# Optimization experiments

Hardware: AMD Instinct MI355X
Metric: run time of the kernel (lower is better)

Reference implementation:

```python
import jax, jax.numpy as jnp
import numpy as np


def phi(x):
    # ELU + 1 feature map (Katharopoulos et al. 2020)
    return jax.nn.elu(x) + 1.0


def setup_inputs() -> dict:
    key = jax.random.key(0)
    k1, k2, k3 = jax.random.split(key, 3)
    B, T, D = 2, 2048, 512
    x = jax.random.normal(k1, (B, T, D), dtype=jnp.float32)
    # torch nn.Linear stores weight as (out_features, in_features)
    w_qkv = jax.random.normal(k2, (3 * D, D), dtype=jnp.float32) * 0.02
    w_out = jax.random.normal(k3, (D, D), dtype=jnp.float32) * 0.02
    return {"x": x, "w_qkv": w_qkv, "w_out": w_out, "n_heads": 16}


def reference(x, w_qkv, w_out, n_heads):
    B, T, D = x.shape
    H = n_heads
    Dh = D // H
    qkv = x @ w_qkv.T                                   # (B,T,3D)
    qkv = qkv.reshape(B, T, 3, H, Dh).transpose(2, 0, 3, 1, 4)  # (3,B,H,T,Dh)
    q, k, v = phi(qkv[0]), phi(qkv[1]), qkv[2]
    # kv outer product: (B,H,T,Dh_k,Dh_v), causal cumsum over time
    kv = k[..., :, None] * v[..., None, :]
    kv_cumsum = jnp.cumsum(kv, axis=2)
    num = jnp.einsum('bhtd,bhtde->bhte', q, kv_cumsum)  # (B,H,T,Dh)
    k_cumsum = jnp.cumsum(k, axis=2)
    denom = jnp.einsum('bhtd,bhtd->bht', q, k_cumsum)[..., None]
    denom = jnp.maximum(denom, 1e-6)
    out = num / denom                                   # (B,H,T,Dh)
    out = out.transpose(0, 2, 1, 3).reshape(B, T, D)
    return out @ w_out.T
```

## Files before the change

### kernel.cpp

```cpp
#include <hip/hip_runtime.h>
#include <math.h>

#define B_ 2
#define T_ 2048
#define D_ 512
#define H_ 16
#define DH 32
#define L_ 64
#define C_ 32
#define BH 32
#define NC 1024
#define VTP 72

typedef __attribute__((ext_vector_type(8))) short bf16x8;
typedef __attribute__((ext_vector_type(4))) float f32x4;
typedef __attribute__((ext_vector_type(4))) unsigned short u16x4;

#define AS1 __attribute__((address_space(1)))
#define AS3 __attribute__((address_space(3)))

__device__ __forceinline__ float bf2f(unsigned short u) {
    union { float f; unsigned int i; } v; v.i = ((unsigned int)u) << 16; return v.f;
}
__device__ __forceinline__ unsigned short f2bf(float f) {
    union { float f; unsigned int u; } v; v.f = f;
    unsigned int u = v.u;
    unsigned int r = u + 0x7FFFu + ((u >> 16) & 1u);
    return (unsigned short)(r >> 16);
}
__device__ __forceinline__ bf16x8 phi_frag(bf16x8 in) {
    bf16x8 r;
    #pragma unroll
    for (int i = 0; i < 8; ++i) {
        float f = bf2f((unsigned short)in[i]);
        f = f > 0.f ? f + 1.f : __expf(f);
        r[i] = (short)f2bf(f);
    }
    return r;
}
__device__ __forceinline__ void gload_lds16(const unsigned short* g, unsigned short* l) {
    __builtin_amdgcn_global_load_lds((const AS1 unsigned int*)g, (AS3 unsigned int*)l, 16, 0, 0);
}

__global__ __launch_bounds__(256) void convert_all(const float* __restrict__ x,
                                                   const float* __restrict__ wq,
                                                   const float* __restrict__ wo,
                                                   unsigned short* __restrict__ xb,
                                                   unsigned short* __restrict__ wqb,
                                                   unsigned short* __restrict__ wob)
{
    int i = blockIdx.x * 256 + threadIdx.x;
    const float* src; unsigned short* dst; int off;
    if (i < 524288)      { src = x;  dst = xb;  off = i; }
    else if (i < 720896) { src = wq; dst = wqb; off = i - 524288; }
    else                 { src = wo; dst = wob; off = i - 720896; }
    float4 v = ((const float4*)src)[off];
    u16x4 o;
    o.x = f2bf(v.x); o.y = f2bf(v.y); o.z = f2bf(v.z); o.w = f2bf(v.w);
    ((u16x4*)dst)[off] = o;
}

template<bool OUT_BF16>
__global__ __launch_bounds__(256) void gemm_bf16_nt(const unsigned short* __restrict__ A,
                                                    const unsigned short* __restrict__ W,
                                                    void* __restrict__ Cout,
                                                    int M, int N, int K)
{
    __shared__ unsigned short As[128][32];
    __shared__ unsigned short Bs[128][32];
    const int tid = threadIdx.x;
    const int lane = tid & 63;
    const int wave = tid >> 6;
    const int wr = wave >> 1;
    const int wc = wave & 1;
    const size_t bm = (size_t)blockIdx.x * 128;
    const size_t bn = (size_t)blockIdx.y * 128;

    const int srow = wave * 32 + (lane >> 2);
    const int scol = (lane & 3) * 8;
    const unsigned short* ag0 = A + (bm + srow) * (size_t)K + scol;
    const unsigned short* ag1 = ag0 + (size_t)16 * K;
    const unsigned short* bg0 = W + (bn + srow) * (size_t)K + scol;
    const unsigned short* bg1 = bg0 + (size_t)16 * K;
    unsigned short* al0 = &As[wave * 32][0];
    unsigned short* al1 = &As[wave * 32 + 16][0];
    unsigned short* bl0 = &Bs[wave * 32][0];
    unsigned short* bl1 = &Bs[wave * 32 + 16][0];

    f32x4 acc[4][4];
    #pragma unroll
    for (int m = 0; m < 4; ++m)
        #pragma unroll
        for (int n = 0; n < 4; ++n)
            acc[m][n] = (f32x4){0.f, 0.f, 0.f, 0.f};

    const int rr = lane & 15;
    const int kb = (lane >> 4) * 8;

    for (int k0 = 0; k0 < K; k0 += 32) {
        gload_lds16(ag0 + k0, al0);
        gload_lds16(ag1 + k0, al1);
        gload_lds16(bg0 + k0, bl0);
        gload_lds16(bg1 + k0, bl1);
        __syncthreads();
        bf16x8 af[4], bfr[4];
        #pragma unroll
        for (int m = 0; m < 4; ++m) af[m] = *(const bf16x8*)&As[wr * 64 + m * 16 + rr][kb];
        #pragma unroll
        for (int n = 0; n < 4; ++n) bfr[n] = *(const bf16x8*)&Bs[wc * 64 + n * 16 + rr][kb];
        #pragma unroll
        for (int m = 0; m < 4; ++m)
            #pragma unroll
            for (int n = 0; n < 4; ++n)
                acc[m][n] = __builtin_amdgcn_mfma_f32_16x16x32_bf16(af[m], bfr[n], acc[m][n], 0, 0, 0);
        __syncthreads();
    }

    const int cr = (lane >> 4) * 4;
    const int cc = lane & 15;
    #pragma unroll
    for (int m = 0; m < 4; ++m)
        #pragma unroll
        for (int n = 0; n < 4; ++n)
            #pragma unroll
            for (int j = 0; j < 4; ++j) {
                size_t row = bm + wr * 64 + m * 16 + cr + j;
                size_t col = bn + wc * 64 + n * 16 + cc;
                float v = acc[m][n][j];
                if (OUT_BF16) ((unsigned short*)Cout)[row * N + col] = f2bf(v);
                else          ((float*)Cout)[row * N + col] = v;
            }
}

__global__ __launch_bounds__(256) void chunk_sum(const unsigned short* __restrict__ qkv,
                                                 float* __restrict__ cSf)
{
    __shared__ unsigned short Kt[4][DH][VTP];
    __shared__ unsigned short Vt[4][48][VTP];
    const int tid = threadIdx.x;
    const int lane = tid & 63;
    const int wave = tid >> 6;
    const int chunk = blockIdx.x * 4 + wave;
    const int c = chunk & 31;
    const int h = (chunk >> 5) & 15;
    const int b = chunk >> 9;
    const size_t rowbase = ((size_t)(b * T_ + c * L_)) * (3 * D_) + h * DH;
    const int half = lane & 1;

    #pragma unroll
    for (int it = 0; it < 2; ++it) {
        int t = (lane >> 1) + it * 32;
        const unsigned short* kp = qkv + rowbase + (size_t)t * (3 * D_) + D_ + half * 16;
        const unsigned short* vp = qkv + rowbase + (size_t)t * (3 * D_) + 2 * D_ + half * 16;
        bf16x8 k0 = phi_frag(*(const bf16x8*)kp);
        bf16x8 k1 = phi_frag(*(const bf16x8*)(kp + 8));
        bf16x8 v0 = *(const bf16x8*)vp;
        bf16x8 v1 = *(const bf16x8*)(vp + 8);
        #pragma unroll
        for (int i = 0; i < 8; ++i) {
            Kt[wave][half * 16 + i][t]     = (unsigned short)k0[i];
            Kt[wave][half * 16 + 8 + i][t] = (unsigned short)k1[i];
            Vt[wave][half * 16 + i][t]     = (unsigned short)v0[i];
            Vt[wave][half * 16 + 8 + i][t] = (unsigned short)v1[i];
        }
    }
    Vt[wave][32][lane] = 0x3F80;

    const int fr = lane & 15;
    const int fg = lane >> 4;
    f32x4 acc[3][2];
    #pragma unroll
    for (int m = 0; m < 3; ++m)
        #pragma unroll
        for (int n = 0; n < 2; ++n)
            acc[m][n] = (f32x4){0.f, 0.f, 0.f, 0.f};

    #pragma unroll
    for (int ks = 0; ks < 2; ++ks) {
        int toff = fg * 8 + ks * 32;
        bf16x8 av[3], bk[2];
        #pragma unroll
        for (int m = 0; m < 3; ++m) av[m] = *(const bf16x8*)&Vt[wave][m * 16 + fr][toff];
        #pragma unroll
        for (int n = 0; n < 2; ++n) bk[n] = *(const bf16x8*)&Kt[wave][n * 16 + fr][toff];
        #pragma unroll
        for (int m = 0; m < 3; ++m)
            #pragma unroll
            for (int n = 0; n < 2; ++n)
                acc[m][n] = __builtin_amdgcn_mfma_f32_16x16x32_bf16(av[m], bk[n], acc[m][n], 0, 0, 0);
    }

    float* outp = cSf + (size_t)chunk * (48 * 32);
    #pragma unroll
    for (int m = 0; m < 2; ++m)
        #pragma unroll
        for (int n = 0; n < 2; ++n)
            #pragma unroll
            for (int r = 0; r < 4; ++r)
                outp[(m * 16 + fg * 4 + r) * 32 + n * 16 + fr] = acc[m][n][r];
    if (fg == 0) {
        #pragma unroll
        for (int n = 0; n < 2; ++n)
            outp[32 * 32 + n * 16 + fr] = acc[2][n][0];
    }
}

__global__ __launch_bounds__(256) void chunk_scan(const float* __restrict__ cSf,
                                                  unsigned short* __restrict__ cSt)
{
    int idx = blockIdx.x * 256 + threadIdx.x;
    int bh = idx / (33 * 32);
    int r  = idx % (33 * 32);
    float acc = 0.f;
    const float* src = cSf + (size_t)bh * C_ * (48 * 32) + r;
    unsigned short* dst = cSt + (size_t)bh * C_ * (48 * 32) + r;
    #pragma unroll 8
    for (int c = 0; c < C_; ++c) {
        dst[(size_t)c * (48 * 32)] = f2bf(acc);
        acc += src[(size_t)c * (48 * 32)];
    }
}

__global__ __launch_bounds__(256) void chunk_out(const unsigned short* __restrict__ qkv,
                                                 const unsigned short* __restrict__ cSt,
                                                 unsigned short* __restrict__ attn)
{
    __shared__ unsigned short Vt[2][48][VTP];
    __shared__ unsigned short Am[4][32][VTP];
    const int tid = threadIdx.x;
    const int lane = tid & 63;
    const int wave = tid >> 6;
    const int ci = wave >> 1;
    const int wh = wave & 1;
    const int chunk = blockIdx.x * 2 + ci;
    const int c = chunk & 31;
    const int h = (chunk >> 5) & 15;
    const int b = chunk >> 9;
    const size_t rowbase = ((size_t)(b * T_ + c * L_)) * (3 * D_) + h * DH;
    const int fr = lane & 15;
    const int fg = lane >> 4;

    {
        int t = wh * 32 + (lane >> 1);
        int half = lane & 1;
        const unsigned short* vp = qkv + rowbase + (size_t)t * (3 * D_) + 2 * D_ + half * 16;
        bf16x8 v0 = *(const bf16x8*)vp;
        bf16x8 v1 = *(const bf16x8*)(vp + 8);
        #pragma unroll
        for (int i = 0; i < 8; ++i) {
            Vt[ci][half * 16 + i][t]     = (unsigned short)v0[i];
            Vt[ci][half * 16 + 8 + i][t] = (unsigned short)v1[i];
        }
        if (half == 0) Vt[ci][32][t] = 0x3F80;
    }

    bf16x8 aq[2];
    #pragma unroll
    for (int mm = 0; mm < 2; ++mm) {
        int m = wh * 2 + mm;
        const unsigned short* qp = qkv + rowbase + (size_t)(m * 16 + fr) * (3 * D_) + fg * 8;
        aq[mm] = phi_frag(*(const bf16x8*)qp);
    }
    bf16x8 bk[4];
    const int nmax = wh * 2 + 1;
    #pragma unroll
    for (int n = 0; n < 4; ++n) {
        if (n <= nmax) {
            const unsigned short* kp = qkv + rowbase + (size_t)(n * 16 + fr) * (3 * D_) + D_ + fg * 8;
            bk[n] = phi_frag(*(const bf16x8*)kp);
        }
    }
    bf16x8 bkv[3];
    #pragma unroll
    for (int n = 0; n < 3; ++n)
        bkv[n] = *(const bf16x8*)&cSt[(size_t)chunk * 1536 + (size_t)(n * 16 + fr) * 32 + fg * 8];

    f32x4 zero = (f32x4){0.f, 0.f, 0.f, 0.f};
    f32x4 acc[2][3];
    #pragma unroll
    for (int mm = 0; mm < 2; ++mm)
        #pragma unroll
        for (int n = 0; n < 3; ++n)
            acc[mm][n] = __builtin_amdgcn_mfma_f32_16x16x32_bf16(aq[mm], bkv[n], zero, 0, 0, 0);

    #pragma unroll
    for (int mm = 0; mm < 2; ++mm) {
        int m = wh * 2 + mm;
        #pragma unroll
        for (int n = 0; n < 4; ++n) {
            if (n <= m) {
                f32x4 s = __builtin_amdgcn_mfma_f32_16x16x32_bf16(aq[mm], bk[n], zero, 0, 0, 0);
                #pragma unroll
                for (int r = 0; r < 4; ++r) {
                    unsigned short v = f2bf(s[r]);
                    if (n == m && fr > fg * 4 + r) v = 0;
                    Am[wave][mm * 16 + fg * 4 + r][n * 16 + fr] = v;
                }
            }
        }
    }
    {
        int zc = wh ? 48 : 16;
        *(uint2*)&Am[wave][fr][zc + fg * 4] = (uint2){0u, 0u};
    }
    __syncthreads();

    #pragma unroll
    for (int ks = 0; ks < 2; ++ks) {
        if (ks <= wh) {
            bf16x8 bv[3];
            #pragma unroll
            for (int n = 0; n < 3; ++n)
                bv[n] = *(const bf16x8*)&Vt[ci][n * 16 + fr][fg * 8 + ks * 32];
            #pragma unroll
            for (int mm = 0; mm < 2; ++mm) {
                bf16x8 aa = *(const bf16x8*)&Am[wave][mm * 16 + fr][fg * 8 + ks * 32];
                #pragma unroll
                for (int n = 0; n < 3; ++n)
                    acc[mm][n] = __builtin_amdgcn_mfma_f32_16x16x32_bf16(aa, bv[n], acc[mm][n], 0, 0, 0);
            }
        }
    }

    #pragma unroll
    for (int mm = 0; mm < 2; ++mm) {
        float dn[4];
        #pragma unroll
        for (int r = 0; r < 4; ++r)
            dn[r] = __shfl(acc[mm][2][r], lane & 48);
        #pragma unroll
        for (int r = 0; r < 4; ++r) {
            float inv = 1.0f / fmaxf(dn[r], 1e-6f);
            #pragma unroll
            for (int n = 0; n < 2; ++n)
                Am[wave][mm * 16 + fg * 4 + r][n * 16 + fr] = f2bf(acc[mm][n][r] * inv);
        }
    }
    {
        int lrow = lane >> 1;
        int half = lane & 1;
        uint4 q0 = *(const uint4*)&Am[wave][lrow][half * 16];
        uint4 q1 = *(const uint4*)&Am[wave][lrow][half * 16 + 8];
        size_t grow = (size_t)(b * T_ + c * L_ + wh * 32 + lrow);
        unsigned short* dst = attn + grow * D_ + h * DH + half * 16;
        *(uint4*)dst = q0;
        *(uint4*)(dst + 8) = q1;
    }
}

extern "C" void kernel_launch(void* const* d_in, const int* in_sizes, int n_in,
                              void* d_out, int out_size, void* d_ws, size_t ws_size,
                              hipStream_t stream) {
    const float* x     = (const float*)d_in[0];
    const float* w_qkv = (const float*)d_in[1];
    const float* w_out = (const float*)d_in[2];
    float* out = (float*)d_out;

    char* ws = (char*)d_ws;
    unsigned short* qkvb  = (unsigned short*)ws;
    unsigned short* attnb = (unsigned short*)(ws + 12582912);
    unsigned short* xb    = (unsigned short*)(ws + 16777216);
    unsigned short* wqb   = (unsigned short*)(ws + 20971520);
    unsigned short* wob   = (unsigned short*)(ws + 22544384);
    float* cSf            = (float*)(ws + 23068672);
    unsigned short* cSt   = (unsigned short*)(ws + 29360128);

    convert_all<<<3072, 256, 0, stream>>>(x, w_qkv, w_out, xb, wqb, wob);

    dim3 g1(4096 / 128, 1536 / 128);
    gemm_bf16_nt<true><<<g1, 256, 0, stream>>>(xb, wqb, qkvb, 4096, 1536, 512);

    chunk_sum<<<NC / 4, 256, 0, stream>>>(qkvb, cSf);
    chunk_scan<<<132, 256, 0, stream>>>(cSf, cSt);
    chunk_out<<<NC / 2, 256, 0, stream>>>(qkvb, cSt, attnb);

    dim3 g2(4096 / 128, 512 / 128);
    gemm_bf16_nt<false><<<g2, 256, 0, stream>>>(attnb, wob, out, 4096, 512, 512);
}
```

Baseline: 55.50 us.

## Fuse chunk prefix scan into chunk_out and use 64-row tiles for output GEMM

Removes the separate chunk_scan kernel: each chunk_out wave now sums the preceding chunks' fp32 state directly from cSf before converting to bf16, trading one launch and a bf16 staging buffer for redundant O(c) reads per chunk. The GEMM is templated on the M tile size, and the output projection uses BM=64, which doubles its block count (256 instead of 128) to fill more CUs. The redundant prefix reads grow with chunk index, so late chunks do up to 31 extra state loads.

```diff
diff --git a/kernel.cpp b/kernel.cpp
--- a/kernel.cpp
+++ b/kernel.cpp
@@ -60,36 +60,35 @@
     ((u16x4*)dst)[off] = o;
 }
 
-template<bool OUT_BF16>
+template<int BM, bool OUT_BF16>
 __global__ __launch_bounds__(256) void gemm_bf16_nt(const unsigned short* __restrict__ A,
                                                     const unsigned short* __restrict__ W,
                                                     void* __restrict__ Cout,
                                                     int M, int N, int K)
 {
-    __shared__ unsigned short As[128][32];
+    constexpr int MF = BM / 32;
+    __shared__ unsigned short As[BM][32];
     __shared__ unsigned short Bs[128][32];
     const int tid = threadIdx.x;
     const int lane = tid & 63;
     const int wave = tid >> 6;
     const int wr = wave >> 1;
     const int wc = wave & 1;
-    const size_t bm = (size_t)blockIdx.x * 128;
+    const size_t bm = (size_t)blockIdx.x * BM;
     const size_t bn = (size_t)blockIdx.y * 128;
 
-    const int srow = wave * 32 + (lane >> 2);
-    const int scol = (lane & 3) * 8;
-    const unsigned short* ag0 = A + (bm + srow) * (size_t)K + scol;
-    const unsigned short* ag1 = ag0 + (size_t)16 * K;
-    const unsigned short* bg0 = W + (bn + srow) * (size_t)K + scol;
+    const int lrow = lane >> 2;
+    const int lcol = (lane & 3) * 8;
+    const unsigned short* ag0 = A + (bm + wave * (BM / 4) + lrow) * (size_t)K + lcol;
+    unsigned short* al0 = &As[wave * (BM / 4)][0];
+    const unsigned short* bg0 = W + (bn + wave * 32 + lrow) * (size_t)K + lcol;
     const unsigned short* bg1 = bg0 + (size_t)16 * K;
-    unsigned short* al0 = &As[wave * 32][0];
-    unsigned short* al1 = &As[wave * 32 + 16][0];
     unsigned short* bl0 = &Bs[wave * 32][0];
     unsigned short* bl1 = &Bs[wave * 32 + 16][0];
 
-    f32x4 acc[4][4];
-    #pragma unroll
-    for (int m = 0; m < 4; ++m)
+    f32x4 acc[MF][4];
+    #pragma unroll
+    for (int m = 0; m < MF; ++m)
         #pragma unroll
         for (int n = 0; n < 4; ++n)
             acc[m][n] = (f32x4){0.f, 0.f, 0.f, 0.f};
@@ -99,17 +98,17 @@
 
     for (int k0 = 0; k0 < K; k0 += 32) {
         gload_lds16(ag0 + k0, al0);
-        gload_lds16(ag1 + k0, al1);
+        if constexpr (BM == 128) gload_lds16(ag0 + (size_t)16 * K + k0, al0 + 16 * 32);
         gload_lds16(bg0 + k0, bl0);
         gload_lds16(bg1 + k0, bl1);
         __syncthreads();
-        bf16x8 af[4], bfr[4];
-        #pragma unroll
-        for (int m = 0; m < 4; ++m) af[m] = *(const bf16x8*)&As[wr * 64 + m * 16 + rr][kb];
+        bf16x8 af[MF], bfr[4];
+        #pragma unroll
+        for (int m = 0; m < MF; ++m) af[m] = *(const bf16x8*)&As[wr * (BM / 2) + m * 16 + rr][kb];
         #pragma unroll
         for (int n = 0; n < 4; ++n) bfr[n] = *(const bf16x8*)&Bs[wc * 64 + n * 16 + rr][kb];
         #pragma unroll
-        for (int m = 0; m < 4; ++m)
+        for (int m = 0; m < MF; ++m)
             #pragma unroll
             for (int n = 0; n < 4; ++n)
                 acc[m][n] = __builtin_amdgcn_mfma_f32_16x16x32_bf16(af[m], bfr[n], acc[m][n], 0, 0, 0);
@@ -119,12 +118,12 @@
     const int cr = (lane >> 4) * 4;
     const int cc = lane & 15;
     #pragma unroll
-    for (int m = 0; m < 4; ++m)
+    for (int m = 0; m < MF; ++m)
         #pragma unroll
         for (int n = 0; n < 4; ++n)
             #pragma unroll
             for (int j = 0; j < 4; ++j) {
-                size_t row = bm + wr * 64 + m * 16 + cr + j;
+                size_t row = bm + wr * (BM / 2) + m * 16 + cr + j;
                 size_t col = bn + wc * 64 + n * 16 + cc;
                 float v = acc[m][n][j];
                 if (OUT_BF16) ((unsigned short*)Cout)[row * N + col] = f2bf(v);
@@ -205,24 +204,8 @@
     }
 }
 
-__global__ __launch_bounds__(256) void chunk_scan(const float* __restrict__ cSf,
-                                                  unsigned short* __restrict__ cSt)
-{
-    int idx = blockIdx.x * 256 + threadIdx.x;
-    int bh = idx / (33 * 32);
-    int r  = idx % (33 * 32);
-    float acc = 0.f;
-    const float* src = cSf + (size_t)bh * C_ * (48 * 32) + r;
-    unsigned short* dst = cSt + (size_t)bh * C_ * (48 * 32) + r;
-    #pragma unroll 8
-    for (int c = 0; c < C_; ++c) {
-        dst[(size_t)c * (48 * 32)] = f2bf(acc);
-        acc += src[(size_t)c * (48 * 32)];
-    }
-}
-
 __global__ __launch_bounds__(256) void chunk_out(const unsigned short* __restrict__ qkv,
-                                                 const unsigned short* __restrict__ cSt,
+                                                 const float* __restrict__ cSf,
                                                  unsigned short* __restrict__ attn)
 {
     __shared__ unsigned short Vt[2][48][VTP];
@@ -254,6 +237,30 @@
         if (half == 0) Vt[ci][32][t] = 0x3F80;
     }
 
+    float pf[3][8];
+    #pragma unroll
+    for (int n = 0; n < 3; ++n)
+        #pragma unroll
+        for (int i = 0; i < 8; ++i) pf[n][i] = 0.f;
+    {
+        const size_t chunkbase = (size_t)(chunk & ~31);
+        for (int j = 0; j < c; ++j) {
+            const float* sp = cSf + (chunkbase + j) * (48 * 32);
+            #pragma unroll
+            for (int n = 0; n < 3; ++n) {
+                f32x4 lo = *(const f32x4*)&sp[(n * 16 + fr) * 32 + fg * 8];
+                f32x4 hi = *(const f32x4*)&sp[(n * 16 + fr) * 32 + fg * 8 + 4];
+                #pragma unroll
+                for (int i = 0; i < 4; ++i) { pf[n][i] += lo[i]; pf[n][4 + i] += hi[i]; }
+            }
+        }
+    }
+    bf16x8 bkv[3];
+    #pragma unroll
+    for (int n = 0; n < 3; ++n)
+        #pragma unroll
+        for (int i = 0; i < 8; ++i) bkv[n][i] = (short)f2bf(pf[n][i]);
+
     bf16x8 aq[2];
     #pragma unroll
     for (int mm = 0; mm < 2; ++mm) {
@@ -270,10 +277,6 @@
             bk[n] = phi_frag(*(const bf16x8*)kp);
         }
     }
-    bf16x8 bkv[3];
-    #pragma unroll
-    for (int n = 0; n < 3; ++n)
-        bkv[n] = *(const bf16x8*)&cSt[(size_t)chunk * 1536 + (size_t)(n * 16 + fr) * 32 + fg * 8];
 
     f32x4 zero = (f32x4){0.f, 0.f, 0.f, 0.f};
     f32x4 acc[2][3];
@@ -363,17 +366,15 @@
     unsigned short* wqb   = (unsigned short*)(ws + 20971520);
     unsigned short* wob   = (unsigned short*)(ws + 22544384);
     float* cSf            = (float*)(ws + 23068672);
-    unsigned short* cSt   = (unsigned short*)(ws + 29360128);
 
     convert_all<<<3072, 256, 0, stream>>>(x, w_qkv, w_out, xb, wqb, wob);
 
     dim3 g1(4096 / 128, 1536 / 128);
-    gemm_bf16_nt<true><<<g1, 256, 0, stream>>>(xb, wqb, qkvb, 4096, 1536, 512);
+    gemm_bf16_nt<128, true><<<g1, 256, 0, stream>>>(xb, wqb, qkvb, 4096, 1536, 512);
 
     chunk_sum<<<NC / 4, 256, 0, stream>>>(qkvb, cSf);
-    chunk_scan<<<132, 256, 0, stream>>>(cSf, cSt);
-    chunk_out<<<NC / 2, 256, 0, stream>>>(qkvb, cSt, attnb);
-
-    dim3 g2(4096 / 128, 512 / 128);
-    gemm_bf16_nt<false><<<g2, 256, 0, stream>>>(attnb, wob, out, 4096, 512, 512);
-}
+    chunk_out<<<NC / 2, 256, 0, stream>>>(qkvb, cSf, attnb);
+
+    dim3 g2(4096 / 64, 512 / 128);
+    gemm_bf16_nt<64, false><<<g2, 256, 0, stream>>>(attnb, wob, out, 4096, 512, 512);
+}
```

After: 87.01 us. 1.57x slower.
